# Kernel tuning notes

Measured on AMD Instinct MI355X. Metric: run time of the kernel, lower is better.

Reference implementation:

```python
import jax, jax.numpy as jnp
import numpy as np

CHAR_NUM = 5000
EMB = 128
RAD_EMB = 64
TOTAL_RAD = 300
HID = 512
CLS = 10
B, T = 64, 512
PAD_ID, START_ID, END_ID = 0, 8, 9
NEG = -10000.0


def setup_inputs() -> dict:
    key = jax.random.key(0)
    ks = jax.random.split(key, 16)
    s = 0.08
    D_in = EMB + RAD_EMB
    inp = {
        "batch_data": jax.random.randint(ks[0], (B, T), 0, CHAR_NUM, dtype=jnp.int32),
        "batch_onerad": jax.random.randint(ks[1], (B, T), 0, TOTAL_RAD, dtype=jnp.int32),
        "batch_tag": jax.random.randint(ks[2], (B, T), 0, START_ID, dtype=jnp.int32),
        "char_emb": jax.random.normal(ks[3], (CHAR_NUM, EMB), jnp.float32) * s,
        "rad_emb": jax.random.normal(ks[4], (TOTAL_RAD, RAD_EMB), jnp.float32) * s,
        "w_ih_f": jax.random.normal(ks[5], (4 * HID, D_in), jnp.float32) * s,
        "w_hh_f": jax.random.normal(ks[6], (4 * HID, HID), jnp.float32) * s,
        "b_f": jax.random.normal(ks[7], (4 * HID,), jnp.float32) * s,
        "w_ih_b": jax.random.normal(ks[8], (4 * HID, D_in), jnp.float32) * s,
        "w_hh_b": jax.random.normal(ks[9], (4 * HID, HID), jnp.float32) * s,
        "b_b": jax.random.normal(ks[10], (4 * HID,), jnp.float32) * s,
        "w_cls": jax.random.normal(ks[11], (CLS, 2 * HID), jnp.float32) * s,
        "b_cls": jax.random.normal(ks[12], (CLS,), jnp.float32) * s,
    }
    # transition[to, from] init per the module's __init__
    trans = np.full((CLS, CLS), 1.0 / CLS, dtype=np.float32)
    trans[START_ID, :] = NEG
    trans[:, END_ID] = NEG
    trans[PAD_ID, END_ID] = 0.05
    inp["transition"] = jnp.asarray(trans)
    return inp


def _run_lstm(xs, w_ih, w_hh, b):
    # xs: [T, B, D] -> hs: [T, B, H]; torch gate order i,f,g,o
    Bsz = xs.shape[1]
    h0 = jnp.zeros((Bsz, HID), xs.dtype)
    c0 = jnp.zeros((Bsz, HID), xs.dtype)

    def step(carry, x_t):
        h, c = carry
        g = x_t @ w_ih.T + h @ w_hh.T + b
        i, f, gg, o = jnp.split(g, 4, axis=-1)
        c = jax.nn.sigmoid(f) * c + jax.nn.sigmoid(i) * jnp.tanh(gg)
        h = jax.nn.sigmoid(o) * jnp.tanh(c)
        return (h, c), h

    _, hs = jax.lax.scan(step, (h0, c0), xs)
    return hs


def _emissions(batch_data, batch_onerad, char_emb, rad_emb,
               w_ih_f, w_hh_f, b_f, w_ih_b, w_hh_b, b_b, w_cls, b_cls):
    emb = jnp.concatenate([char_emb[batch_data], rad_emb[batch_onerad]], axis=2)  # [B,T,D]
    # dropout in eval mode == identity
    xs = jnp.transpose(emb, (1, 0, 2))  # [T,B,D]
    hs_f = _run_lstm(xs, w_ih_f, w_hh_f, b_f)
    hs_b = _run_lstm(xs[::-1], w_ih_b, w_hh_b, b_b)[::-1]
    hs = jnp.concatenate([hs_f, hs_b], axis=-1)  # [T,B,2H]
    emission = hs @ w_cls.T + b_cls  # [T,B,C]
    return jnp.transpose(emission, (1, 0, 2))  # [B,T,C]


def _forward_alg(feats, transition):
    # feats: [B,T,C]; CRF partition function per batch element
    Bsz, _, C = feats.shape
    alpha0 = jnp.full((C, Bsz), NEG, feats.dtype).at[START_ID, :].set(0.0)
    feats_t = jnp.transpose(feats, (1, 2, 0))  # [T, C(to), B]

    def step(alpha, feat_t):
        # aa[to, from, b]
        aa = alpha[None, :, :] + feat_t[:, None, :] + transition[:, :, None]
        return jax.nn.logsumexp(aa, axis=1), None

    alpha, _ = jax.lax.scan(step, alpha0, feats_t)
    return jax.nn.logsumexp(alpha, axis=0)  # [B]


def _score_sentence(feats, tags, transition):
    # feats: [B,T,C], tags: [B,T]
    Bsz = feats.shape[0]
    start = jnp.full((Bsz, 1), START_ID, tags.dtype)
    tags_ext = jnp.concatenate([start, tags], axis=1)  # [B,T+1]
    trans_sc = transition[tags_ext[:, 1:], tags_ext[:, :-1]].sum(axis=1)  # [B]
    emit_sc = jnp.take_along_axis(feats, tags[:, :, None], axis=2)[..., 0].sum(axis=1)
    return trans_sc + emit_sc  # [B]


def reference(batch_data, batch_onerad, batch_tag, char_emb, rad_emb,
              w_ih_f, w_hh_f, b_f, w_ih_b, w_hh_b, b_b, w_cls, b_cls, transition):
    feats = _emissions(batch_data, batch_onerad, char_emb, rad_emb,
                       w_ih_f, w_hh_f, b_f, w_ih_b, w_hh_b, b_b, w_cls, b_cls)
    fwd = _forward_alg(feats, transition)
    gold = _score_sentence(feats, batch_tag, transition)
    Bsz = feats.shape[0]
    loss = (fwd.sum() - gold.sum()) / Bsz
    return loss
```

## Files before the change

### kernel.cpp

```cpp
#include <hip/hip_runtime.h>

typedef unsigned short u16;
typedef unsigned int u32;
typedef float f32x16 __attribute__((ext_vector_type(16)));
typedef float f32x4v __attribute__((ext_vector_type(4)));
typedef unsigned int u32x4 __attribute__((ext_vector_type(4)));
typedef unsigned int u32x2 __attribute__((ext_vector_type(2)));

#define TT 512
#define NBLK 64

static const size_t OFF_EMBX = 0;
static const size_t OFF_HS   = 12582912;
static const size_t OFF_HBUF = 79691776;
static const size_t OFF_BAR  = 79953920;
static const size_t OFF_FEAT = 79954176;
static const size_t OFF_RES  = 81264896;
static const size_t WS_NEED  = 81265152;

__device__ inline u32 packbf(float a, float b) {
  u32 ua = __float_as_uint(a); ua += 0x7fffu + ((ua >> 16) & 1u);
  u32 ub = __float_as_uint(b); ub += 0x7fffu + ((ub >> 16) & 1u);
  return (ua >> 16) | (ub & 0xffff0000u);
}
__device__ inline u16 f2b(float a) {
  u32 u = __float_as_uint(a); u += 0x7fffu + ((u >> 16) & 1u);
  return (u16)(u >> 16);
}
__device__ inline float sigm(float x) { return 1.f / (1.f + __expf(-x)); }
__device__ inline float tanhx(float x) {
  float e = __expf(-2.f * fabsf(x));
  float t = (1.f - e) / (1.f + e);
  return (x < 0.f) ? -t : t;
}

__device__ inline u32x4 ldg_cc(const u16* p) {
  u32x4 r;
  asm volatile("global_load_dwordx4 %0, %1, off sc0 sc1"
               : "=v"(r) : "v"(p) : "memory");
  return r;
}
__device__ inline int ldflag(const int* p) {
  int r;
  asm volatile("global_load_dword %0, %1, off sc0 sc1"
               : "=v"(r) : "v"(p) : "memory");
  asm volatile("s_waitcnt vmcnt(0)" ::: "memory");
  return r;
}
__device__ inline void stg_at8(u16* p, u32x2 v) {
  asm volatile("global_atomic_swap_x2 %0, %1, off sc1"
               :: "v"(p), "v"(v) : "memory");
}
__device__ inline void stflag_at(int* p, int v) {
  asm volatile("global_atomic_swap %0, %1, off sc1"
               :: "v"(p), "v"(v) : "memory");
}

__global__ __launch_bounds__(256) void k_embed(const int* __restrict__ bdata,
                                               const int* __restrict__ brad,
                                               const float* __restrict__ cemb,
                                               const float* __restrict__ remb,
                                               u16* __restrict__ embX) {
  int t = blockIdx.x;
  int tid = threadIdx.x;
#pragma unroll
  for (int r = 0; r < 6; ++r) {
    int cc = r * 256 + tid;
    int b = cc / 24;
    int j = cc - b * 24;
    int ic = bdata[b * TT + t];
    int ir = brad[b * TT + t];
    const float* src = (j < 16) ? (cemb + (size_t)ic * 128 + j * 8)
                                : (remb + (size_t)ir * 64 + (j - 16) * 8);
    f32x4v f0 = *(const f32x4v*)src;
    f32x4v f1 = *(const f32x4v*)(src + 4);
    u32x4 o;
    o[0] = packbf(f0[0], f0[1]); o[1] = packbf(f0[2], f0[3]);
    o[2] = packbf(f1[0], f1[1]); o[3] = packbf(f1[2], f1[3]);
    *(u32x4*)(embX + ((size_t)t * 64 + b) * 192 + j * 8) = o;
  }
}

__global__ __launch_bounds__(256, 1) void k_lstm(
    const u16* __restrict__ embX, u16* __restrict__ hbuf, u16* __restrict__ hs,
    const float* __restrict__ wihf, const float* __restrict__ whhf, const float* __restrict__ bf,
    const float* __restrict__ wihb, const float* __restrict__ whhb, const float* __restrict__ bb,
    int* __restrict__ flags) {
  __shared__ u16 smh[64 * 512];
  __shared__ u16 hl[64 * 16];

  const int tid = threadIdx.x;
  const int lane = tid & 63;
  const int wid = tid >> 6;
  const int blk = blockIdx.x;
  const int dir = blk >> 5;
  const int j0 = (blk & 31) << 4;

  const float* wih = dir ? wihb : wihf;
  const float* whh = dir ? whhb : whhf;
  const float* bias = dir ? bb : bf;

  const int m = wid >> 1, n = wid & 1;
  const int l31 = lane & 31;
  const int hi = lane >> 5;

  const int gate = l31 >> 3;
  const int jloc = (l31 & 7) + 8 * m;
  const int grow = gate * 512 + j0 + jloc;
  const float* pih = wih + (size_t)grow * 192 + 8 * hi;
  const float* phh = whh + (size_t)grow * 512 + 8 * hi;
  u32x4 aw[44];
#pragma unroll
  for (int kt = 0; kt < 44; ++kt) {
    const float* p = (kt < 12) ? (pih + kt * 16) : (phh + (kt - 12) * 16);
    f32x4v f0 = *(const f32x4v*)p;
    f32x4v f1 = *(const f32x4v*)(p + 4);
    u32x4 a;
    a[0] = packbf(f0[0], f0[1]); a[1] = packbf(f0[2], f0[3]);
    a[2] = packbf(f1[0], f1[1]); a[3] = packbf(f1[2], f1[3]);
    aw[kt] = a;
  }

  u16* hb_dT = hbuf + dir * 65536;

  const int bb_ = n * 32 + l31;
  const int swzr = (bb_ & 15) << 4;
  const char* hbase = (const char*)smh + bb_ * 1024;
  const int hoff = hi * 16;

  const int jme = j0 + 8 * m + 4 * hi;
  float creg[4] = {0.f, 0.f, 0.f, 0.f};
  float bI[4], bF[4], bG[4], bO[4];
#pragma unroll
  for (int q = 0; q < 4; ++q) {
    bI[q] = bias[jme + q];
    bF[q] = bias[512 + jme + q];
    bG[q] = bias[1024 + jme + q];
    bO[q] = bias[1536 + jme + q];
  }

  int* myflags = flags + dir * 64;

  for (int t = 0; t < TT; ++t) {
    const int par = t & 1;
    const int tx = dir ? (511 - t) : t;

    u32x4 xf[12];
    const u16* xbase = embX + ((size_t)tx * 64 + bb_) * 192 + 8 * hi;
#pragma unroll
    for (int kt = 0; kt < 12; ++kt) xf[kt] = *(const u32x4*)(xbase + kt * 16);

    if (t) {
      if (wid == 0) {
        int f = ldflag(myflags + (lane & 31) * 2);
        int guard = 0;
        while (__any(f < t)) {
          if (++guard > 200000) break;
          f = ldflag(myflags + (lane & 31) * 2);
        }
      }
      __syncthreads();
    }

    {
      const u16* src = hb_dT + par * 32768;
      u32x4 v[16];
#pragma unroll
      for (int r = 0; r < 16; ++r) {
        int b = r * 4 + wid;
        v[r] = ldg_cc(src + b * 512 + lane * 8);
      }
      asm volatile("s_waitcnt vmcnt(0)" ::: "memory");
#pragma unroll
      for (int r = 0; r < 16; ++r) {
        int b = r * 4 + wid;
        int kk = (lane * 8) ^ ((b & 15) << 3);
        *(u32x4*)(smh + b * 512 + kk) = v[r];
      }
    }
    __syncthreads();

    f32x16 acc;
#pragma unroll
    for (int i = 0; i < 16; ++i) acc[i] = 0.f;
    asm volatile("s_nop 7\ns_nop 7");
#pragma unroll
    for (int kt = 0; kt < 32; ++kt) {
      u32x4 bfrag = *(const u32x4*)(hbase + ((kt * 32 + hoff) ^ swzr));
      asm("v_mfma_f32_32x32x16_bf16 %0, %1, %2, %0" : "+v"(acc) : "v"(aw[kt]), "v"(bfrag));
    }
#pragma unroll
    for (int kt = 0; kt < 12; ++kt) {
      asm("v_mfma_f32_32x32x16_bf16 %0, %1, %2, %0" : "+v"(acc) : "v"(aw[32 + kt]), "v"(xf[kt]));
    }
    asm volatile("s_nop 7\ns_nop 7\ns_nop 7");

    {
      u16* dstT = hb_dT + (par ^ 1) * 32768;
      u32 hp0 = 0, hp1 = 0;
#pragma unroll
      for (int q = 0; q < 4; ++q) {
        float gi = acc[q] + bI[q];
        float gf = acc[4 + q] + bF[q];
        float gg = acc[8 + q] + bG[q];
        float go = acc[12 + q] + bO[q];
        float cn = sigm(gf) * creg[q] + sigm(gi) * tanhx(gg);
        creg[q] = cn;
        float h = sigm(go) * tanhx(cn);
        u32 h16 = (u32)f2b(h);
        if (q == 0) hp0 = h16;
        else if (q == 1) hp0 |= h16 << 16;
        else if (q == 2) hp1 = h16;
        else hp1 |= h16 << 16;
      }
      u32x2 hv; hv[0] = hp0; hv[1] = hp1;
      stg_at8(dstT + bb_ * 512 + jme, hv);
      *(u32x2*)(hl + bb_ * 16 + (jme - j0)) = hv;
    }

    asm volatile("s_waitcnt vmcnt(0)" ::: "memory");
    __syncthreads();
    if (t != TT - 1 && tid == 0) stflag_at(myflags + (blk & 31) * 2, t + 1);
    if (tid < 128) {
      int ob = tid >> 1, hf = tid & 1;
      u32x4 v = *(const u32x4*)(hl + ob * 16 + hf * 8);
      *(u32x4*)(hs + ((size_t)tx * 64 + ob) * 1024 + dir * 512 + j0 + hf * 8) = v;
    }
  }
}

__global__ __launch_bounds__(256) void k_emis(const u16* __restrict__ hs,
                                              const float* __restrict__ wcls,
                                              const float* __restrict__ bcls,
                                              float* __restrict__ feats) {
  __shared__ float wl[10240];
  int tid = threadIdx.x;
  for (int i = tid; i < 10240; i += 256) wl[i] = wcls[i];
  __syncthreads();
  int row = blockIdx.x * 256 + tid;
  const u16* hrow = hs + (size_t)row * 1024;
  float acc[10];
#pragma unroll
  for (int c = 0; c < 10; ++c) acc[c] = bcls[c];
  for (int k0 = 0; k0 < 1024; k0 += 8) {
    u32x4 v = *(const u32x4*)(hrow + k0);
    float x0 = __uint_as_float(v[0] << 16);
    float x1 = __uint_as_float(v[0] & 0xffff0000u);
    float x2 = __uint_as_float(v[1] << 16);
    float x3 = __uint_as_float(v[1] & 0xffff0000u);
    float x4 = __uint_as_float(v[2] << 16);
    float x5 = __uint_as_float(v[2] & 0xffff0000u);
    float x6 = __uint_as_float(v[3] << 16);
    float x7 = __uint_as_float(v[3] & 0xffff0000u);
#pragma unroll
    for (int c = 0; c < 10; ++c) {
      const float* w = &wl[c * 1024 + k0];
      f32x4v wa = *(const f32x4v*)w;
      f32x4v wb = *(const f32x4v*)(w + 4);
      acc[c] += x0 * wa[0] + x1 * wa[1] + x2 * wa[2] + x3 * wa[3] +
                x4 * wb[0] + x5 * wb[1] + x6 * wb[2] + x7 * wb[3];
    }
  }
#pragma unroll
  for (int c = 0; c < 10; ++c) feats[(size_t)row * 10 + c] = acc[c];
}

__global__ void k_crf(const float* __restrict__ feats, const float* __restrict__ trans,
                      const int* __restrict__ btag, float* __restrict__ res) {
  int b = blockIdx.x;
  int lane = threadIdx.x;
  float tr[10];
  int to = lane < 10 ? lane : 9;
#pragma unroll
  for (int f = 0; f < 10; ++f) tr[f] = trans[to * 10 + f];
  float al[10];
#pragma unroll
  for (int f = 0; f < 10; ++f) al[f] = (f == 8) ? 0.f : -10000.f;
  float fe_next = (lane < 10) ? feats[(size_t)b * 10 + lane] : 0.f;
  for (int t = 0; t < 512; ++t) {
    float fe = fe_next;
    if (t < 511)
      fe_next = (lane < 10) ? feats[((size_t)(t + 1) * 64 + b) * 10 + lane] : 0.f;
    float mx = -3.0e38f;
#pragma unroll
    for (int f = 0; f < 10; ++f) mx = fmaxf(mx, al[f] + tr[f]);
    float s = 0.f;
#pragma unroll
    for (int f = 0; f < 10; ++f) s += __expf(al[f] + tr[f] - mx);
    float an = mx + __logf(s) + fe;
#pragma unroll
    for (int f = 0; f < 10; ++f) al[f] = __shfl(an, f);
  }
  float mx = -3.0e38f;
#pragma unroll
  for (int f = 0; f < 10; ++f) mx = fmaxf(mx, al[f]);
  float s = 0.f;
#pragma unroll
  for (int f = 0; f < 10; ++f) s += __expf(al[f] - mx);
  float fwd = mx + __logf(s);
  float g = 0.f;
  for (int t = lane; t < 512; t += 64) {
    int tg = btag[b * 512 + t];
    int pv = (t == 0) ? 8 : btag[b * 512 + t - 1];
    g += trans[tg * 10 + pv] + feats[((size_t)t * 64 + b) * 10 + tg];
  }
#pragma unroll
  for (int off = 32; off > 0; off >>= 1) g += __shfl_down(g, off);
  if (lane == 0) res[b] = fwd - g;
}

__global__ void k_fin(const float* __restrict__ res, float* __restrict__ out) {
  float v = res[threadIdx.x];
#pragma unroll
  for (int off = 32; off > 0; off >>= 1) v += __shfl_down(v, off);
  if (threadIdx.x == 0) out[0] = v * (1.f / 64.f);
}

extern "C" void kernel_launch(void* const* d_in, const int* in_sizes, int n_in,
                              void* d_out, int out_size, void* d_ws, size_t ws_size,
                              hipStream_t stream) {
  (void)in_sizes; (void)n_in; (void)out_size;
  if (ws_size < WS_NEED) return;

  const int* bdata = (const int*)d_in[0];
  const int* brad  = (const int*)d_in[1];
  const int* btag  = (const int*)d_in[2];
  const float* cemb = (const float*)d_in[3];
  const float* remb = (const float*)d_in[4];
  const float* wihf = (const float*)d_in[5];
  const float* whhf = (const float*)d_in[6];
  const float* bf   = (const float*)d_in[7];
  const float* wihb = (const float*)d_in[8];
  const float* whhb = (const float*)d_in[9];
  const float* bb   = (const float*)d_in[10];
  const float* wcls = (const float*)d_in[11];
  const float* bcls = (const float*)d_in[12];
  const float* trans = (const float*)d_in[13];

  char* ws = (char*)d_ws;
  u16* embX = (u16*)(ws + OFF_EMBX);
  u16* hs   = (u16*)(ws + OFF_HS);
  u16* hbuf = (u16*)(ws + OFF_HBUF);
  int* flags = (int*)(ws + OFF_BAR);
  float* feats = (float*)(ws + OFF_FEAT);
  float* res = (float*)(ws + OFF_RES);

  hipMemsetAsync(ws + OFF_HBUF, 0, 262144 + 512, stream);

  k_embed<<<512, 256, 0, stream>>>(bdata, brad, cemb, remb, embX);
  k_lstm<<<64, 256, 0, stream>>>(embX, hbuf, hs, wihf, whhf, bf, wihb, whhb, bb, flags);
  k_emis<<<128, 256, 0, stream>>>(hs, wcls, bcls, feats);
  k_crf<<<64, 64, 0, stream>>>(feats, trans, btag, res);
  k_fin<<<1, 64, 0, stream>>>(res, (float*)d_out);
}
```

Measured before the change: 2.841 ms.

## Pin each LSTM direction to one XCD and sync through L2 instead of atomics

The persistent LSTM kernel now launches 512 blocks and reads the hardware XCC id. Blocks on XCDs other than 0 and 1 exit at once, and each block on XCD 0 or 1 claims a hidden-unit slot with an atomic counter, so every direction runs on a single XCD. Because all producers and consumers of a direction then share one L2, the per-step h exchange and the flag stores and loads drop the system-coherent atomics (sc1) and use plain sc0 stores and loads. This is meant to cut cross-die coherence latency in the serial recurrence, but it relies on the undocumented XCD id and on at least 32 blocks per direction being co-resident on one XCD, which risks a hang or wrong results if scheduling differs.

```diff
diff --git a/kernel.cpp b/kernel.cpp
--- a/kernel.cpp
+++ b/kernel.cpp
@@ -8,7 +8,6 @@
 typedef unsigned int u32x2 __attribute__((ext_vector_type(2)));
 
 #define TT 512
-#define NBLK 64
 
 static const size_t OFF_EMBX = 0;
 static const size_t OFF_HS   = 12582912;
@@ -23,10 +22,6 @@
   u32 ub = __float_as_uint(b); ub += 0x7fffu + ((ub >> 16) & 1u);
   return (ua >> 16) | (ub & 0xffff0000u);
 }
-__device__ inline u16 f2b(float a) {
-  u32 u = __float_as_uint(a); u += 0x7fffu + ((u >> 16) & 1u);
-  return (u16)(u >> 16);
-}
 __device__ inline float sigm(float x) { return 1.f / (1.f + __expf(-x)); }
 __device__ inline float tanhx(float x) {
   float e = __expf(-2.f * fabsf(x));
@@ -34,25 +29,25 @@
   return (x < 0.f) ? -t : t;
 }
 
-__device__ inline u32x4 ldg_cc(const u16* p) {
+__device__ inline u32x4 ldg_l2(const u16* p) {
   u32x4 r;
-  asm volatile("global_load_dwordx4 %0, %1, off sc0 sc1"
+  asm volatile("global_load_dwordx4 %0, %1, off sc0"
                : "=v"(r) : "v"(p) : "memory");
   return r;
 }
+__device__ inline void stg8_l2(u16* p, u32x2 v) {
+  asm volatile("global_store_dwordx2 %0, %1, off sc0"
+               :: "v"(p), "v"(v) : "memory");
+}
 __device__ inline int ldflag(const int* p) {
   int r;
-  asm volatile("global_load_dword %0, %1, off sc0 sc1"
+  asm volatile("global_load_dword %0, %1, off sc0"
                : "=v"(r) : "v"(p) : "memory");
   asm volatile("s_waitcnt vmcnt(0)" ::: "memory");
   return r;
 }
-__device__ inline void stg_at8(u16* p, u32x2 v) {
-  asm volatile("global_atomic_swap_x2 %0, %1, off sc1"
-               :: "v"(p), "v"(v) : "memory");
-}
-__device__ inline void stflag_at(int* p, int v) {
-  asm volatile("global_atomic_swap %0, %1, off sc1"
+__device__ inline void stflag(int* p, int v) {
+  asm volatile("global_store_dword %0, %1, off sc0"
                :: "v"(p), "v"(v) : "memory");
 }
 
@@ -88,13 +83,25 @@
     int* __restrict__ flags) {
   __shared__ u16 smh[64 * 512];
   __shared__ u16 hl[64 * 16];
+  __shared__ int s_slot;
 
   const int tid = threadIdx.x;
+
+  int xcd;
+  asm volatile("s_getreg_b32 %0, hwreg(20, 0, 32)" : "=s"(xcd));
+  xcd &= 15;
+  if (xcd >= 2) return;
+  const int dir = xcd;
+
+  int* claim = flags + 128;
+  if (tid == 0) s_slot = atomicAdd(&claim[dir], 1);
+  __syncthreads();
+  const int slot = s_slot;
+  if (slot >= 32) return;
+  const int j0 = slot << 4;
+
   const int lane = tid & 63;
   const int wid = tid >> 6;
-  const int blk = blockIdx.x;
-  const int dir = blk >> 5;
-  const int j0 = (blk & 31) << 4;
 
   const float* wih = dir ? wihb : wihf;
   const float* whh = dir ? whhb : whhf;
@@ -155,7 +162,7 @@
         int f = ldflag(myflags + (lane & 31) * 2);
         int guard = 0;
         while (__any(f < t)) {
-          if (++guard > 200000) break;
+          if (++guard > 400000) break;
           f = ldflag(myflags + (lane & 31) * 2);
         }
       }
@@ -168,7 +175,7 @@
 #pragma unroll
       for (int r = 0; r < 16; ++r) {
         int b = r * 4 + wid;
-        v[r] = ldg_cc(src + b * 512 + lane * 8);
+        v[r] = ldg_l2(src + b * 512 + lane * 8);
       }
       asm volatile("s_waitcnt vmcnt(0)" ::: "memory");
 #pragma unroll
@@ -207,20 +214,21 @@
         float cn = sigm(gf) * creg[q] + sigm(gi) * tanhx(gg);
         creg[q] = cn;
         float h = sigm(go) * tanhx(cn);
-        u32 h16 = (u32)f2b(h);
+        u32 u = __float_as_uint(h); u += 0x7fffu + ((u >> 16) & 1u);
+        u32 h16 = u >> 16;
         if (q == 0) hp0 = h16;
         else if (q == 1) hp0 |= h16 << 16;
         else if (q == 2) hp1 = h16;
         else hp1 |= h16 << 16;
       }
       u32x2 hv; hv[0] = hp0; hv[1] = hp1;
-      stg_at8(dstT + bb_ * 512 + jme, hv);
+      stg8_l2(dstT + bb_ * 512 + jme, hv);
       *(u32x2*)(hl + bb_ * 16 + (jme - j0)) = hv;
     }
 
     asm volatile("s_waitcnt vmcnt(0)" ::: "memory");
     __syncthreads();
-    if (t != TT - 1 && tid == 0) stflag_at(myflags + (blk & 31) * 2, t + 1);
+    if (t != TT - 1 && tid == 0) stflag(myflags + slot * 2, t + 1);
     if (tid < 128) {
       int ob = tid >> 1, hf = tid & 1;
       u32x4 v = *(const u32x4*)(hl + ob * 16 + hf * 8);
@@ -345,10 +353,10 @@
   float* feats = (float*)(ws + OFF_FEAT);
   float* res = (float*)(ws + OFF_RES);
 
-  hipMemsetAsync(ws + OFF_HBUF, 0, 262144 + 512, stream);
+  hipMemsetAsync(ws + OFF_HBUF, 0, 262144 + 768, stream);
 
   k_embed<<<512, 256, 0, stream>>>(bdata, brad, cemb, remb, embX);
-  k_lstm<<<64, 256, 0, stream>>>(embX, hbuf, hs, wihf, whhf, bf, wihb, whhb, bb, flags);
+  k_lstm<<<512, 256, 0, stream>>>(embX, hbuf, hs, wihf, whhf, bf, wihb, whhb, bb, flags);
   k_emis<<<128, 256, 0, stream>>>(hs, wcls, bcls, feats);
   k_crf<<<64, 64, 0, stream>>>(feats, trans, btag, res);
   k_fin<<<1, 64, 0, stream>>>(res, (float*)d_out);
```

Result: faster. 2.593 ms (-8.7%).
